# Optimization experiments

Hardware: AMD Instinct MI355X
Metric: run time of the kernel (lower is better)

## Reference

```python
import jax, jax.numpy as jnp
import numpy as np

BS, C_IN, H, W = 16, 128, 64, 64
C_OUT, K, STRIDE, PAD, DIL = 256, 3, 1, 1, 1
ALPHA = 0.5  # scaling_factor
QMAX = 127.0  # int8 symmetric fake-quant


def _fake_quant(t):
    # symmetric per-tensor int8 fake quantization with straight-through estimator
    s = jax.lax.stop_gradient(jnp.max(jnp.abs(t))) / QMAX
    s = jnp.where(s == 0, 1.0, s)
    q = jnp.clip(jnp.round(t / s), -QMAX, QMAX) * s
    return t + jax.lax.stop_gradient(q - t)  # STE


def setup_inputs() -> dict:
    key = jax.random.key(0)
    k1, k2, k3 = jax.random.split(key, 3)
    x = jax.random.normal(k1, (BS, C_IN, H, W), dtype=jnp.float32)
    weight = jax.random.normal(k2, (C_OUT, C_IN, K, K), dtype=jnp.float32) * 0.05
    bias = jax.random.normal(k3, (C_OUT,), dtype=jnp.float32) * 0.01
    return {"x": x, "weight": weight, "bias": bias}


def reference(x, weight, bias):
    bs, _, h_in, w_in = x.shape
    ickhkw = C_IN * K * K
    h_out = (h_in + 2 * PAD - DIL * (K - 1) - 1) // STRIDE + 1
    w_out = (w_in + 2 * PAD - DIL * (K - 1) - 1) // STRIDE + 1

    # im2col (matches torch F.unfold feature ordering: channel-major, then kh, kw)
    patches = jax.lax.conv_general_dilated_patches(
        x, filter_shape=(K, K), window_strides=(STRIDE, STRIDE),
        padding=((PAD, PAD), (PAD, PAD)), rhs_dilation=(DIL, DIL),
    )  # [bs, ickhkw, h_out, w_out]
    cols = patches.reshape(bs, ickhkw, h_out * w_out)
    cols = cols.transpose(0, 2, 1).reshape(-1, ickhkw)  # [bs*L, ickhkw]

    w2 = weight.reshape(C_OUT, ickhkw)

    # SmoothQuant per-column scales (detached)
    w_scale = jax.lax.stop_gradient(jnp.max(jnp.abs(w2), axis=0))    # [ickhkw]
    act_scale = jax.lax.stop_gradient(jnp.max(jnp.abs(cols), axis=0))  # [ickhkw]
    scale = act_scale ** ALPHA / w_scale ** (1.0 - ALPHA)
    scale = jnp.where(scale == 0, 1.0, scale)

    w_s = _fake_quant(w2 * scale)
    x_s = _fake_quant(cols / scale)

    out = x_s @ w_s.T  # [bs*L, C_OUT]
    out = out.reshape(bs, h_out * w_out, C_OUT).transpose(0, 2, 1)
    out = out.reshape(bs, C_OUT, h_out, w_out)
    return out + bias.reshape(1, C_OUT, 1, 1)
```

## Files before the change

### kernel.cpp

```cpp
#include <hip/hip_runtime.h>
#include <cstdint>

#define C_IN   128
#define C_OUT  256
#define KK     1152
#define NPIX   4096
#define BS     16
#define M_ROWS 65536
#define QMAXF  127.0f

typedef int v4i __attribute__((ext_vector_type(4)));

#define OFF_QW    75497472
#define OFF_SCALE 75792384
#define OFF_QMUL  75796992
#define OFF_APART 75801600
#define OFF_SCAL  75843072

__global__ void k_prep(const float* __restrict__ x, const float* __restrict__ wgt,
                       float* __restrict__ act_part, float* __restrict__ w_part) {
    const int tid = threadIdx.x;
    if (blockIdx.x >= 1024) {
        int t = blockIdx.x - 1024;
        int j = (t % 5) * 256 + tid;
        int s = t / 5;
        if (j >= KK) return;
        const float* p = wgt + (size_t)s * 16 * KK + j;
        float m = 0.f;
#pragma unroll
        for (int i = 0; i < 16; i++) m = fmaxf(m, fabsf(p[(size_t)i * KK]));
        w_part[s * KK + j] = m;
        return;
    }
    const int c = blockIdx.x >> 3, s = blockIdx.x & 7;
    float m[9];
#pragma unroll
    for (int i = 0; i < 9; i++) m[i] = 0.f;
    for (int p = tid; p < 2 * NPIX; p += 256) {
        int b = s * 2 + (p >> 12);
        int hw = p & 4095;
        int h = hw >> 6, w = hw & 63;
        float v = fabsf(x[b * (C_IN * NPIX) + c * NPIX + hw]);
        bool rr[3] = { h <= 62, true, h >= 1 };
        bool cc[3] = { w <= 62, true, w >= 1 };
#pragma unroll
        for (int i = 0; i < 3; i++)
#pragma unroll
            for (int jq = 0; jq < 3; jq++)
                m[i * 3 + jq] = fmaxf(m[i * 3 + jq], (rr[i] && cc[jq]) ? v : 0.f);
    }
    __shared__ float sm[9][4];
    int lane = tid & 63, wid = tid >> 6;
#pragma unroll
    for (int i = 0; i < 9; i++) {
        float v = m[i];
        for (int off = 32; off > 0; off >>= 1) v = fmaxf(v, __shfl_down(v, off));
        if (lane == 0) sm[i][wid] = v;
    }
    __syncthreads();
    if (tid < 9) {
        float v = fmaxf(fmaxf(sm[tid][0], sm[tid][1]), fmaxf(sm[tid][2], sm[tid][3]));
        act_part[s * KK + c * 9 + tid] = v;
    }
}

__global__ void k_scales(const float* __restrict__ act_part, const float* __restrict__ w_part,
                         float* __restrict__ scale, float* __restrict__ qmul,
                         float* __restrict__ scalars) {
    const int tid = threadIdx.x;
    float sc_local[2] = {1.f, 1.f};
    float mx = 0.f, mw = 0.f;
#pragma unroll
    for (int t = 0; t < 2; t++) {
        int j = tid + t * 1024;
        if (j < KK) {
            float a = 0.f;
#pragma unroll
            for (int s = 0; s < 8; s++) a = fmaxf(a, act_part[s * KK + j]);
            float wv = 0.f;
#pragma unroll
            for (int s = 0; s < 16; s++) wv = fmaxf(wv, w_part[s * KK + j]);
            float sc = sqrtf(a) / sqrtf(wv);
            if (sc == 0.f) sc = 1.0f;
            scale[j] = sc;
            sc_local[t] = sc;
            mx = fmaxf(mx, a / sc);
            mw = fmaxf(mw, wv * sc);
        }
    }
    __shared__ float smx[16], smw[16];
    __shared__ float s_x_sh;
    int lane = tid & 63, wid = tid >> 6;
    for (int off = 32; off > 0; off >>= 1) {
        mx = fmaxf(mx, __shfl_down(mx, off));
        mw = fmaxf(mw, __shfl_down(mw, off));
    }
    if (lane == 0) { smx[wid] = mx; smw[wid] = mw; }
    __syncthreads();
    if (tid == 0) {
        float a = 0.f, b = 0.f;
        for (int i = 0; i < 16; i++) { a = fmaxf(a, smx[i]); b = fmaxf(b, smw[i]); }
        float s_x = a / QMAXF; if (s_x == 0.f) s_x = 1.f;
        float s_w = b / QMAXF; if (s_w == 0.f) s_w = 1.f;
        scalars[0] = s_x; scalars[1] = s_w; scalars[2] = s_x * s_w;
        s_x_sh = s_x;
    }
    __syncthreads();
    float s_x = s_x_sh;
#pragma unroll
    for (int t = 0; t < 2; t++) {
        int j = tid + t * 1024;
        if (j < KK) qmul[j] = 1.0f / (sc_local[t] * s_x);
    }
}

#define QX_LDSROW 292
__global__ __launch_bounds__(256) void k_quant(const float* __restrict__ x,
                                               const float* __restrict__ wgt,
                                               const float* __restrict__ scale,
                                               const float* __restrict__ qmul,
                                               const float* __restrict__ scalars,
                                               signed char* __restrict__ qA,
                                               signed char* __restrict__ qW) {
    const int tid = threadIdx.x;
    if (blockIdx.x >= 2048) {
        int idx = (blockIdx.x - 2048) * 256 + tid;
        int j = idx % KK;
        float s_w = scalars[1];
        float t = wgt[idx] * scale[j];
        float q = rintf(t / s_w);
        q = fminf(fmaxf(q, -QMAXF), QMAXF);
        qW[idx] = (signed char)(int)q;
        return;
    }
    __shared__ float qm[288];
    __shared__ signed char ob[128 * QX_LDSROW];
    const int qt  = blockIdx.x & 3;
    const int rp  = (blockIdx.x >> 2) & 31;
    const int b   = blockIdx.x >> 7;
    const int c0  = qt * 32;
    const int oh0 = rp * 2;

    for (int i = tid; i < 288; i += 256) qm[i] = qmul[c0 * 9 + i];
    __syncthreads();

    const int lane = tid & 63, wv = tid >> 6;
    const float* xb = x + (size_t)b * (C_IN * NPIX);

    for (int it = 0; it < 16; it++) {
        int pair = wv + 4 * it;
        int c = pair >> 1;
        int oh = oh0 + (pair & 1);
        const float* xp = xb + (c0 + c) * NPIX + oh * 64 + lane;
        float xm = (oh >= 1)  ? xp[-64] : 0.f;
        float x0 = xp[0];
        float xq = (oh <= 62) ? xp[64]  : 0.f;
        float xm_l = __shfl_up(xm, 1);  if (lane == 0)  xm_l = 0.f;
        float xm_r = __shfl_down(xm, 1); if (lane == 63) xm_r = 0.f;
        float x0_l = __shfl_up(x0, 1);  if (lane == 0)  x0_l = 0.f;
        float x0_r = __shfl_down(x0, 1); if (lane == 63) x0_r = 0.f;
        float xq_l = __shfl_up(xq, 1);  if (lane == 0)  xq_l = 0.f;
        float xq_r = __shfl_down(xq, 1); if (lane == 63) xq_r = 0.f;
        float win[9] = { xm_l, xm, xm_r, x0_l, x0, x0_r, xq_l, xq, xq_r };
        signed char* orow = ob + ((oh - oh0) * 64 + lane) * QX_LDSROW + c * 9;
#pragma unroll
        for (int t = 0; t < 9; t++) {
            float q = rintf(win[t] * qm[c * 9 + t]);
            q = fminf(fmaxf(q, -QMAXF), QMAXF);
            orow[t] = (signed char)(int)q;
        }
    }
    __syncthreads();

    const int r0 = b * NPIX + oh0 * 64;
    for (int idx = tid; idx < 128 * 72; idx += 256) {
        int px = (unsigned)idx / 72u;
        int q  = idx - px * 72;
        int v  = *(const int*)(ob + px * QX_LDSROW + q * 4);
        *(int*)(qA + (size_t)(r0 + px) * KK + c0 * 9 + q * 4) = v;
    }
}

__global__ __launch_bounds__(512) void k_gemm(const signed char* __restrict__ qW,
                                              const signed char* __restrict__ qA,
                                              const float* __restrict__ scalars,
                                              const float* __restrict__ bias,
                                              float* __restrict__ out) {
    __shared__ __align__(16) signed char As[256 * 128];
    __shared__ __align__(16) signed char Bs[128 * 128];
    const int tid = threadIdx.x;
    const int lane = tid & 63, wvid = tid >> 6;
    const int wm = wvid & 3, wn = wvid >> 2;
    const int blockN = blockIdx.x;

    const int r8 = lane >> 3;
    const int cp = (lane & 7) ^ r8;
    const int swz = lane & 7;

    v4i acc[4][4];
#pragma unroll
    for (int i = 0; i < 4; i++)
#pragma unroll
        for (int jq = 0; jq < 4; jq++) acc[i][jq] = (v4i){0, 0, 0, 0};

    for (int k0 = 0; k0 < KK; k0 += 128) {
#pragma unroll
        for (int i = 0; i < 6; i++) {
            int ch = wvid * 6 + i;
            const signed char* src;
            signed char* dst;
            if (ch < 32) {
                src = qW + (size_t)(ch * 8 + r8) * KK + k0 + cp * 16;
                dst = As + ch * 1024;
            } else {
                int cb = ch - 32;
                src = qA + ((size_t)blockN * 128 + cb * 8 + r8) * KK + k0 + cp * 16;
                dst = Bs + cb * 1024;
            }
            __builtin_amdgcn_global_load_lds(
                (const __attribute__((address_space(1))) void*)src,
                (__attribute__((address_space(3))) void*)dst, 16, 0, 0);
        }
        __syncthreads();
#pragma unroll
        for (int h = 0; h < 2; h++) {
            v4i af[4], bf[4];
            const int q4 = (h * 4 + (lane >> 4));
#pragma unroll
            for (int t = 0; t < 4; t++) {
                af[t] = *(const v4i*)(As + (wm * 64 + t * 16 + (lane & 15)) * 128 + (q4 ^ swz) * 16);
                bf[t] = *(const v4i*)(Bs + (wn * 64 + t * 16 + (lane & 15)) * 128 + (q4 ^ swz) * 16);
            }
#pragma unroll
            for (int mt = 0; mt < 4; mt++)
#pragma unroll
                for (int nt = 0; nt < 4; nt++)
                    acc[mt][nt] = __builtin_amdgcn_mfma_i32_16x16x64_i8(af[mt], bf[nt], acc[mt][nt], 0, 0, 0);
        }
        __syncthreads();
    }

    const float ssp = scalars[2];
    const int quad = lane >> 4, col = lane & 15;
    float bv[4][4];
#pragma unroll
    for (int mt = 0; mt < 4; mt++)
#pragma unroll
        for (int rg = 0; rg < 4; rg++)
            bv[mt][rg] = bias[wm * 64 + mt * 16 + quad * 4 + rg];

#pragma unroll
    for (int mt = 0; mt < 4; mt++) {
#pragma unroll
        for (int nt = 0; nt < 4; nt++) {
            int n_g = blockN * 128 + wn * 64 + nt * 16 + col;
            int b = n_g >> 12, pix = n_g & 4095;
#pragma unroll
            for (int rg = 0; rg < 4; rg++) {
                int m_g = wm * 64 + mt * 16 + quad * 4 + rg;
                float v = (float)acc[mt][nt][rg] * ssp + bv[mt][rg];
                out[(size_t)(b * C_OUT + m_g) * NPIX + pix] = v;
            }
        }
    }
}

extern "C" void kernel_launch(void* const* d_in, const int* in_sizes, int n_in,
                              void* d_out, int out_size, void* d_ws, size_t ws_size,
                              hipStream_t stream) {
    const float* x    = (const float*)d_in[0];
    const float* wgt  = (const float*)d_in[1];
    const float* bias = (const float*)d_in[2];
    float* out = (float*)d_out;

    char* ws = (char*)d_ws;
    signed char* qA = (signed char*)ws;
    signed char* qW = (signed char*)(ws + OFF_QW);
    float* w_part   = (float*)(ws + OFF_QW);
    float* scale    = (float*)(ws + OFF_SCALE);
    float* qmul     = (float*)(ws + OFF_QMUL);
    float* act_part = (float*)(ws + OFF_APART);
    float* scalars  = (float*)(ws + OFF_SCAL);

    k_prep<<<1104, 256, 0, stream>>>(x, wgt, act_part, w_part);
    k_scales<<<1, 1024, 0, stream>>>(act_part, w_part, scale, qmul, scalars);
    k_quant<<<2048 + KK, 256, 0, stream>>>(x, wgt, scale, qmul, scalars, qA, qW);
    k_gemm<<<M_ROWS / 128, 512, 0, stream>>>(qW, qA, scalars, bias, out);
}
```

Baseline: 173.1 us.

## Fuse activation im2col quantization into GEMM and reorder K by tap

Removes the separate activation quantization kernel and its 75MB int8 im2col buffer. The GEMM now builds each B tile on the fly from fp32 input, quantizing with per-column multipliers. The K dimension is permuted to tap-major order, with weights quantized into the matching layout, so each 128-wide K slice is one tap across all channels. Each block rereads fp32 input nine times, once per tap, and does quantization arithmetic inside the GEMM loop with no prefetch overlap, trading HBM traffic for more in-kernel latency.

```diff
diff --git a/kernel.cpp b/kernel.cpp
--- a/kernel.cpp
+++ b/kernel.cpp
@@ -10,6 +10,7 @@
 #define QMAXF  127.0f
 
 typedef int v4i __attribute__((ext_vector_type(4)));
+typedef float f4 __attribute__((ext_vector_type(4)));
 
 #define OFF_QW    75497472
 #define OFF_SCALE 75792384
@@ -114,88 +115,48 @@
     }
 }
 
-#define QX_LDSROW 292
-__global__ __launch_bounds__(256) void k_quant(const float* __restrict__ x,
-                                               const float* __restrict__ wgt,
-                                               const float* __restrict__ scale,
-                                               const float* __restrict__ qmul,
-                                               const float* __restrict__ scalars,
-                                               signed char* __restrict__ qA,
-                                               signed char* __restrict__ qW) {
-    const int tid = threadIdx.x;
-    if (blockIdx.x >= 2048) {
-        int idx = (blockIdx.x - 2048) * 256 + tid;
-        int j = idx % KK;
-        float s_w = scalars[1];
-        float t = wgt[idx] * scale[j];
-        float q = rintf(t / s_w);
-        q = fminf(fmaxf(q, -QMAXF), QMAXF);
-        qW[idx] = (signed char)(int)q;
-        return;
-    }
-    __shared__ float qm[288];
-    __shared__ signed char ob[128 * QX_LDSROW];
-    const int qt  = blockIdx.x & 3;
-    const int rp  = (blockIdx.x >> 2) & 31;
-    const int b   = blockIdx.x >> 7;
-    const int c0  = qt * 32;
-    const int oh0 = rp * 2;
-
-    for (int i = tid; i < 288; i += 256) qm[i] = qmul[c0 * 9 + i];
-    __syncthreads();
-
-    const int lane = tid & 63, wv = tid >> 6;
-    const float* xb = x + (size_t)b * (C_IN * NPIX);
-
-    for (int it = 0; it < 16; it++) {
-        int pair = wv + 4 * it;
-        int c = pair >> 1;
-        int oh = oh0 + (pair & 1);
-        const float* xp = xb + (c0 + c) * NPIX + oh * 64 + lane;
-        float xm = (oh >= 1)  ? xp[-64] : 0.f;
-        float x0 = xp[0];
-        float xq = (oh <= 62) ? xp[64]  : 0.f;
-        float xm_l = __shfl_up(xm, 1);  if (lane == 0)  xm_l = 0.f;
-        float xm_r = __shfl_down(xm, 1); if (lane == 63) xm_r = 0.f;
-        float x0_l = __shfl_up(x0, 1);  if (lane == 0)  x0_l = 0.f;
-        float x0_r = __shfl_down(x0, 1); if (lane == 63) x0_r = 0.f;
-        float xq_l = __shfl_up(xq, 1);  if (lane == 0)  xq_l = 0.f;
-        float xq_r = __shfl_down(xq, 1); if (lane == 63) xq_r = 0.f;
-        float win[9] = { xm_l, xm, xm_r, x0_l, x0, x0_r, xq_l, xq, xq_r };
-        signed char* orow = ob + ((oh - oh0) * 64 + lane) * QX_LDSROW + c * 9;
-#pragma unroll
-        for (int t = 0; t < 9; t++) {
-            float q = rintf(win[t] * qm[c * 9 + t]);
-            q = fminf(fmaxf(q, -QMAXF), QMAXF);
-            orow[t] = (signed char)(int)q;
-        }
-    }
-    __syncthreads();
-
-    const int r0 = b * NPIX + oh0 * 64;
-    for (int idx = tid; idx < 128 * 72; idx += 256) {
-        int px = (unsigned)idx / 72u;
-        int q  = idx - px * 72;
-        int v  = *(const int*)(ob + px * QX_LDSROW + q * 4);
-        *(int*)(qA + (size_t)(r0 + px) * KK + c0 * 9 + q * 4) = v;
-    }
-}
-
-__global__ __launch_bounds__(512) void k_gemm(const signed char* __restrict__ qW,
-                                              const signed char* __restrict__ qA,
+__global__ void k_quant_w(const float* __restrict__ wgt, const float* __restrict__ scale,
+                          const float* __restrict__ scalars, signed char* __restrict__ qWp) {
+    int idx = blockIdx.x * 256 + threadIdx.x;
+    int m  = (unsigned)idx / KK;
+    int kp = idx - m * KK;
+    int tap = kp >> 7, c = kp & 127;
+    int j = c * 9 + tap;
+    float s_w = scalars[1];
+    float t = wgt[m * KK + j] * scale[j];
+    float q = rintf(t / s_w);
+    q = fminf(fmaxf(q, -QMAXF), QMAXF);
+    qWp[idx] = (signed char)(int)q;
+}
+
+__global__ __launch_bounds__(512) void k_gemm(const signed char* __restrict__ qWp,
+                                              const float* __restrict__ x,
+                                              const float* __restrict__ qmul,
                                               const float* __restrict__ scalars,
                                               const float* __restrict__ bias,
                                               float* __restrict__ out) {
     __shared__ __align__(16) signed char As[256 * 128];
     __shared__ __align__(16) signed char Bs[128 * 128];
+    __shared__ float qm[KK];
     const int tid = threadIdx.x;
-    const int lane = tid & 63, wvid = tid >> 6;
-    const int wm = wvid & 3, wn = wvid >> 2;
-    const int blockN = blockIdx.x;
+    const int lane = tid & 63, wv = tid >> 6;
+    const int wm = wv & 3, wn = wv >> 2;
+    const int b   = blockIdx.x >> 5;
+    const int rp  = blockIdx.x & 31;
+    const int oh0 = rp * 2;
+    const float* xb = x + (size_t)b * (C_IN * NPIX);
+
+    for (int i = tid; i < KK; i += 512) {
+        int tap = i >> 7, c = i & 127;
+        qm[i] = qmul[c * 9 + tap];
+    }
 
     const int r8 = lane >> 3;
-    const int cp = (lane & 7) ^ r8;
+    const int cpA = (lane & 7) ^ r8;
+    const int ohl = wv & 1;
+    const int px  = ohl * 64 + lane;
     const int swz = lane & 7;
+    const int oh  = oh0 + ohl;
 
     v4i acc[4][4];
 #pragma unroll
@@ -203,33 +164,56 @@
 #pragma unroll
         for (int jq = 0; jq < 4; jq++) acc[i][jq] = (v4i){0, 0, 0, 0};
 
-    for (int k0 = 0; k0 < KK; k0 += 128) {
-#pragma unroll
-        for (int i = 0; i < 6; i++) {
-            int ch = wvid * 6 + i;
-            const signed char* src;
-            signed char* dst;
-            if (ch < 32) {
-                src = qW + (size_t)(ch * 8 + r8) * KK + k0 + cp * 16;
-                dst = As + ch * 1024;
-            } else {
-                int cb = ch - 32;
-                src = qA + ((size_t)blockN * 128 + cb * 8 + r8) * KK + k0 + cp * 16;
-                dst = Bs + cb * 1024;
-            }
+    __syncthreads();
+
+    for (int tap = 0; tap < 9; tap++) {
+        const int kh = (tap * 11) >> 5;
+        const int kw = tap - kh * 3;
+        const int ih = oh + kh - 1;
+        const bool rowok = (unsigned)ih < 64u;
+#pragma unroll
+        for (int i = 0; i < 4; i++) {
+            int ch = wv * 4 + i;
+            const signed char* src = qWp + (size_t)(ch * 8 + r8) * KK + tap * 128 + cpA * 16;
             __builtin_amdgcn_global_load_lds(
                 (const __attribute__((address_space(1))) void*)src,
-                (__attribute__((address_space(3))) void*)dst, 16, 0, 0);
+                (__attribute__((address_space(3))) void*)(As + ch * 1024), 16, 0, 0);
+        }
+        const int iw = lane + kw - 1;
+        const bool colok = (unsigned)iw < 64u;
+        const float* srow = xb + ih * 64 + iw;
+#pragma unroll
+        for (int j = 0; j < 2; j++) {
+            int cc = j * 4 + (wv >> 1);
+            int c0 = cc * 16;
+            int pk[4];
+#pragma unroll
+            for (int d = 0; d < 4; d++) {
+                f4 qv = *(const f4*)(qm + tap * 128 + c0 + d * 4);
+                int w = 0;
+#pragma unroll
+                for (int e = 0; e < 4; e++) {
+                    int c = c0 + d * 4 + e;
+                    float v = (rowok && colok) ? srow[(size_t)c * NPIX] : 0.f;
+                    float q = rintf(v * qv[e]);
+                    q = fminf(fmaxf(q, -QMAXF), QMAXF);
+                    w |= ((int)q & 255) << (8 * e);
+                }
+                pk[d] = w;
+            }
+            *(v4i*)(Bs + px * 128 + ((cc ^ swz) * 16)) = (v4i){pk[0], pk[1], pk[2], pk[3]};
         }
         __syncthreads();
 #pragma unroll
         for (int h = 0; h < 2; h++) {
+            const int q4 = h * 4 + (lane >> 4);
             v4i af[4], bf[4];
-            const int q4 = (h * 4 + (lane >> 4));
 #pragma unroll
             for (int t = 0; t < 4; t++) {
-                af[t] = *(const v4i*)(As + (wm * 64 + t * 16 + (lane & 15)) * 128 + (q4 ^ swz) * 16);
-                bf[t] = *(const v4i*)(Bs + (wn * 64 + t * 16 + (lane & 15)) * 128 + (q4 ^ swz) * 16);
+                int ra = wm * 64 + t * 16 + (lane & 15);
+                af[t] = *(const v4i*)(As + ra * 128 + ((q4 ^ (ra & 7)) * 16));
+                int rb = wn * 64 + t * 16 + (lane & 15);
+                bf[t] = *(const v4i*)(Bs + rb * 128 + ((q4 ^ (rb & 7)) * 16));
             }
 #pragma unroll
             for (int mt = 0; mt < 4; mt++)
@@ -253,13 +237,12 @@
     for (int mt = 0; mt < 4; mt++) {
 #pragma unroll
         for (int nt = 0; nt < 4; nt++) {
-            int n_g = blockN * 128 + wn * 64 + nt * 16 + col;
-            int b = n_g >> 12, pix = n_g & 4095;
+            int n = wn * 64 + nt * 16 + col;
 #pragma unroll
             for (int rg = 0; rg < 4; rg++) {
-                int m_g = wm * 64 + mt * 16 + quad * 4 + rg;
+                int m = wm * 64 + mt * 16 + quad * 4 + rg;
                 float v = (float)acc[mt][nt][rg] * ssp + bv[mt][rg];
-                out[(size_t)(b * C_OUT + m_g) * NPIX + pix] = v;
+                out[(size_t)(b * C_OUT + m) * NPIX + oh0 * 64 + n] = v;
             }
         }
     }
@@ -274,16 +257,15 @@
     float* out = (float*)d_out;
 
     char* ws = (char*)d_ws;
-    signed char* qA = (signed char*)ws;
-    signed char* qW = (signed char*)(ws + OFF_QW);
-    float* w_part   = (float*)(ws + OFF_QW);
-    float* scale    = (float*)(ws + OFF_SCALE);
-    float* qmul     = (float*)(ws + OFF_QMUL);
-    float* act_part = (float*)(ws + OFF_APART);
-    float* scalars  = (float*)(ws + OFF_SCAL);
+    signed char* qWp = (signed char*)(ws + OFF_QW);
+    float* w_part    = (float*)(ws + OFF_QW);
+    float* scale     = (float*)(ws + OFF_SCALE);
+    float* qmul      = (float*)(ws + OFF_QMUL);
+    float* act_part  = (float*)(ws + OFF_APART);
+    float* scalars   = (float*)(ws + OFF_SCAL);
 
     k_prep<<<1104, 256, 0, stream>>>(x, wgt, act_part, w_part);
     k_scales<<<1, 1024, 0, stream>>>(act_part, w_part, scale, qmul, scalars);
-    k_quant<<<2048 + KK, 256, 0, stream>>>(x, wgt, scale, qmul, scalars, qA, qW);
-    k_gemm<<<M_ROWS / 128, 512, 0, stream>>>(qW, qA, scalars, bias, out);
-}
+    k_quant_w<<<(C_OUT * KK) / 256, 256, 0, stream>>>(wgt, scale, scalars, qWp);
+    k_gemm<<<BS * 32, 512, 0, stream>>>(qWp, x, qmul, scalars, bias, out);
+}
```

After: 164.2 us. 1.05x faster.
